# Kernel tuning notes

Hardware: AMD Instinct MI355X
Metric: run time of the kernel (lower is better)

The kernel has to match this reference:

```python
import jax, jax.numpy as jnp
import numpy as np

HEAD_SIZE = 128

def setup_inputs() -> dict:
    key = jax.random.key(0)
    ks = jax.random.split(key, 4)
    B, T, C, H = 8, 2048, 1024, HEAD_SIZE
    x = jax.random.normal(ks[0], (B, T, C), dtype=jnp.float32)
    Wk = jax.random.normal(ks[1], (C, H), dtype=jnp.float32) * (C ** -0.5)
    Wq = jax.random.normal(ks[2], (C, H), dtype=jnp.float32) * (C ** -0.5)
    Wv = jax.random.normal(ks[3], (C, H), dtype=jnp.float32) * (C ** -0.5)
    return {"x": x, "Wk": Wk, "Wq": Wq, "Wv": Wv}

def reference(x, Wk, Wq, Wv):
    # x: [B,T,C]; projections to [B,T,H]
    k = jnp.einsum('btc,ch->bth', x, Wk)
    q = jnp.einsum('btc,ch->bth', x, Wq)
    v = jnp.einsum('btc,ch->bth', x, Wv)
    scale = HEAD_SIZE ** -0.5
    wei = jnp.einsum('bqh,bkh->bqk', q, k) * scale  # [B,T,T]
    T = x.shape[1]
    causal = jnp.tril(jnp.ones((T, T), dtype=bool))
    wei = jnp.where(causal, wei, -jnp.inf)
    wei = jax.nn.softmax(wei, axis=-1)
    # dropout p=0 (eval) -> identity
    out = jnp.einsum('bqk,bkh->bqh', wei, v)  # [B,T,H]
    return out
```

## Files before the change

### kernel.cpp

```cpp
#include <hip/hip_runtime.h>

#define B_DIM 8
#define T_DIM 2048
#define C_DIM 1024
#define H_DIM 128

typedef __attribute__((ext_vector_type(8))) short bf16x8;
typedef __attribute__((ext_vector_type(4))) float f32x4;

__device__ __forceinline__ short f2bf(float f) {
  union { float f; unsigned u; } v; v.f = f;
  unsigned u = v.u;
  unsigned r = (u + 0x7FFFu + ((u >> 16) & 1u)) >> 16;
  return (short)r;
}

__device__ __forceinline__ void gload_lds16(const short* g, short* l) {
  __builtin_amdgcn_global_load_lds(
      (const __attribute__((address_space(1))) void*)g,
      (__attribute__((address_space(3))) void*)l, 16, 0, 0);
}

__device__ __forceinline__ float rowmax16(float x) {
  union { float f; int i; } a, t;
  a.f = x;
  t.i = __builtin_amdgcn_update_dpp(a.i, a.i, 0x128, 0xf, 0xf, false);
  a.f = fmaxf(a.f, t.f);
  t.i = __builtin_amdgcn_update_dpp(a.i, a.i, 0x124, 0xf, 0xf, false);
  a.f = fmaxf(a.f, t.f);
  t.i = __builtin_amdgcn_update_dpp(a.i, a.i, 0x122, 0xf, 0xf, false);
  a.f = fmaxf(a.f, t.f);
  t.i = __builtin_amdgcn_update_dpp(a.i, a.i, 0x121, 0xf, 0xf, false);
  a.f = fmaxf(a.f, t.f);
  return a.f;
}
__device__ __forceinline__ float rowsum16(float x) {
  union { float f; int i; } a, t;
  a.f = x;
  t.i = __builtin_amdgcn_update_dpp(a.i, a.i, 0x128, 0xf, 0xf, false);
  a.f += t.f;
  t.i = __builtin_amdgcn_update_dpp(a.i, a.i, 0x124, 0xf, 0xf, false);
  a.f += t.f;
  t.i = __builtin_amdgcn_update_dpp(a.i, a.i, 0x122, 0xf, 0xf, false);
  a.f += t.f;
  t.i = __builtin_amdgcn_update_dpp(a.i, a.i, 0x121, 0xf, 0xf, false);
  a.f += t.f;
  return a.f;
}

#define NXE ((B_DIM * T_DIM * C_DIM) / 8)
#define NWE ((3 * C_DIM * H_DIM) / 8)

__global__ __launch_bounds__(256) void prep_kernel(
    const float* __restrict__ x, const float* __restrict__ Wk,
    const float* __restrict__ Wq, const float* __restrict__ Wv,
    short* __restrict__ xb, short* __restrict__ Wt) {
  int gid = blockIdx.x * 256 + threadIdx.x;
  if (gid < NXE) {
    const float* src = x + (size_t)gid * 8;
    float4 f0 = ((const float4*)src)[0];
    float4 f1 = ((const float4*)src)[1];
    __attribute__((aligned(16))) short t[8];
    t[0] = f2bf(f0.x); t[1] = f2bf(f0.y); t[2] = f2bf(f0.z); t[3] = f2bf(f0.w);
    t[4] = f2bf(f1.x); t[5] = f2bf(f1.y); t[6] = f2bf(f1.z); t[7] = f2bf(f1.w);
    ((int4*)xb)[gid] = *(const int4*)t;
  } else {
    int j = gid - NXE;
    if (j >= NWE) return;
    int w = j >> 14;
    int r = j & 16383;
    int h = r >> 7;
    int c0 = (r & 127) * 8;
    const float* W = (w == 0) ? Wk : ((w == 1) ? Wq : Wv);
    __attribute__((aligned(16))) short t[8];
#pragma unroll
    for (int i = 0; i < 8; i++) t[i] = f2bf(W[(size_t)(c0 + i) * H_DIM + h]);
    *(int4*)(Wt + (size_t)w * (C_DIM * H_DIM) + h * C_DIM + c0) = *(const int4*)t;
  }
}

__global__ __launch_bounds__(256) void proj_kernel(
    const short* __restrict__ xb, const short* __restrict__ Wt,
    short* __restrict__ Kp, short* __restrict__ Qb, short* __restrict__ Vp) {
  const int wi = blockIdx.y;
  const int m0 = blockIdx.x * 128;
  __shared__ short As[128 * 32];
  __shared__ short Bs[128 * 32];
  const int tid  = threadIdx.x;
  const int lane = tid & 63;
  const int wv   = tid >> 6;
  const int n    = lane & 15;
  const int quad = lane >> 4;
  const int mbase = (wv >> 1) * 64;
  const int nbase = (wv & 1) * 64;
  const short* Wp = Wt + (size_t)wi * (C_DIM * H_DIM);

  const int lr = lane >> 2;
  const int lc = (lane & 3) * 8;

  f32x4 acc[4][4];
#pragma unroll
  for (int i = 0; i < 4; i++)
#pragma unroll
    for (int j = 0; j < 4; j++) {
      f32x4 z = {0.f, 0.f, 0.f, 0.f};
      acc[i][j] = z;
    }

  for (int k0 = 0; k0 < C_DIM; k0 += 32) {
    __syncthreads();
#pragma unroll
    for (int h = 0; h < 2; h++) {
      int ch = wv * 2 + h;
      int row = ch * 16 + lr;
      gload_lds16(xb + (size_t)(m0 + row) * C_DIM + k0 + lc, &As[ch * 512]);
      gload_lds16(Wp + (size_t)row * C_DIM + k0 + lc, &Bs[ch * 512]);
    }
    __syncthreads();

    bf16x8 aF[4], bF[4];
#pragma unroll
    for (int mt = 0; mt < 4; mt++)
      aF[mt] = *(const bf16x8*)&As[(mbase + mt * 16 + n) * 32 + quad * 8];
#pragma unroll
    for (int nt = 0; nt < 4; nt++)
      bF[nt] = *(const bf16x8*)&Bs[(nbase + nt * 16 + n) * 32 + quad * 8];
#pragma unroll
    for (int mt = 0; mt < 4; mt++)
#pragma unroll
      for (int nt = 0; nt < 4; nt++)
        acc[mt][nt] = __builtin_amdgcn_mfma_f32_16x16x32_bf16(
            aF[mt], bF[nt], acc[mt][nt], 0, 0, 0);
  }

#pragma unroll
  for (int mt = 0; mt < 4; mt++) {
#pragma unroll
    for (int nt = 0; nt < 4; nt++) {
#pragma unroll
      for (int i = 0; i < 4; i++) {
        int row = m0 + mbase + mt * 16 + quad * 4 + i;
        int col = nbase + nt * 16 + n;
        short v = f2bf(acc[mt][nt][i]);
        int bb = row >> 11;
        int t  = row & (T_DIM - 1);
        int tt = t >> 6;
        if (wi == 0) {
          int rr = t & 63;
          int knt = rr >> 4, kn = rr & 15;
          int kc = col >> 5, kq = (col >> 3) & 3, kj = col & 7;
          Kp[(((size_t)(bb * 32 + tt) * 16 + knt * 4 + kc) * 512) +
             (kq * 16 + kn) * 8 + kj] = v;
        } else if (wi == 1) {
          Qb[(size_t)row * H_DIM + col] = v;
        } else {
          int vkc = (t >> 5) & 1, vq = (t >> 3) & 3, vj = t & 7;
          int ht = col >> 4, vn = col & 15;
          Vp[(((size_t)(bb * 32 + tt) * 16 + ht * 2 + vkc) * 512) +
             (vq * 16 + vn) * 8 + vj] = v;
        }
      }
    }
  }
}

__global__ __launch_bounds__(256, 4) void attn_kernel(
    const short* __restrict__ Qb, const short* __restrict__ Kp,
    const short* __restrict__ Vp, float* __restrict__ out) {
  const int id = blockIdx.y * 128 + blockIdx.x;
  const int b  = id & 7;
  const int qt = id >> 3;
  const int q0 = qt * 16;
  const int tid  = threadIdx.x;
  const int lane = tid & 63;
  const int g    = tid >> 6;
  const int n    = lane & 15;
  const int quad = lane >> 4;

  __shared__ short Ps[4][16][72];
  __shared__ float Om[16][128];
  __shared__ float Ml[16][2];

  const int ntiles = (qt >> 2) + 1;
  const float scale = 0.08838834764831845f;
  const int row0 = q0 + quad * 4;

  const short* Kbase = Kp + (size_t)b * 32 * 16 * 512;
  const short* Vbase = Vp + (size_t)b * 32 * 16 * 512;

  bf16x8 aQ[4];
  {
    const short* qrow = Qb + (size_t)(b * T_DIM + q0 + n) * H_DIM;
#pragma unroll
    for (int kc = 0; kc < 4; kc++)
      aQ[kc] = *(const bf16x8*)(qrow + kc * 32 + quad * 8);
  }

  f32x4 accO[8];
#pragma unroll
  for (int i = 0; i < 8; i++) {
    f32x4 z = {0.f, 0.f, 0.f, 0.f};
    accO[i] = z;
  }
  float mrow[4] = {-1e30f, -1e30f, -1e30f, -1e30f};
  float lrow[4] = {0.f, 0.f, 0.f, 0.f};

  for (int t = g; t < ntiles; t += 4) {
    const int j0 = t * 64;
    const short* Kt = Kbase + (size_t)t * 16 * 512 + lane * 8;
    const short* Vt = Vbase + (size_t)t * 16 * 512 + lane * 8;
    f32x4 accS[4];
#pragma unroll
    for (int nt = 0; nt < 4; nt++) {
      f32x4 z = {0.f, 0.f, 0.f, 0.f};
      accS[nt] = z;
    }
    bf16x8 fr[8];
#pragma unroll
    for (int nt = 0; nt < 2; nt++)
#pragma unroll
      for (int kc = 0; kc < 4; kc++)
        fr[nt * 4 + kc] = *(const bf16x8*)(Kt + (nt * 4 + kc) * 512);
    __builtin_amdgcn_sched_barrier(0);
#pragma unroll
    for (int nt = 0; nt < 2; nt++)
#pragma unroll
      for (int kc = 0; kc < 4; kc++)
        accS[nt] = __builtin_amdgcn_mfma_f32_16x16x32_bf16(
            aQ[kc], fr[nt * 4 + kc], accS[nt], 0, 0, 0);
    __builtin_amdgcn_sched_barrier(0);
#pragma unroll
    for (int nt = 0; nt < 2; nt++)
#pragma unroll
      for (int kc = 0; kc < 4; kc++)
        fr[nt * 4 + kc] = *(const bf16x8*)(Kt + ((nt + 2) * 4 + kc) * 512);
    __builtin_amdgcn_sched_barrier(0);
#pragma unroll
    for (int nt = 0; nt < 2; nt++)
#pragma unroll
      for (int kc = 0; kc < 4; kc++)
        accS[nt + 2] = __builtin_amdgcn_mfma_f32_16x16x32_bf16(
            aQ[kc], fr[nt * 4 + kc], accS[nt + 2], 0, 0, 0);
    __builtin_amdgcn_sched_barrier(0);

    float mt4[4] = {-1e30f, -1e30f, -1e30f, -1e30f};
#pragma unroll
    for (int nt = 0; nt < 4; nt++) {
      int col = j0 + nt * 16 + n;
#pragma unroll
      for (int i = 0; i < 4; i++) {
        float s = accS[nt][i] * scale;
        s = (col > row0 + i) ? -1e30f : s;
        accS[nt][i] = s;
        mt4[i] = fmaxf(mt4[i], s);
      }
    }
#pragma unroll
    for (int i = 0; i < 4; i++) mt4[i] = rowmax16(mt4[i]);

    bf16x8 frv[8];
#pragma unroll
    for (int ht = 0; ht < 4; ht++)
#pragma unroll
      for (int kc = 0; kc < 2; kc++)
        frv[ht * 2 + kc] = *(const bf16x8*)(Vt + (ht * 2 + kc) * 512);
    __builtin_amdgcn_sched_barrier(0);

    float alpha[4], rsum[4];
#pragma unroll
    for (int i = 0; i < 4; i++) {
      float mnew = fmaxf(mrow[i], mt4[i]);
      alpha[i] = __expf(mrow[i] - mnew);
      mrow[i] = mnew;
      rsum[i] = 0.f;
    }
#pragma unroll
    for (int nt = 0; nt < 4; nt++)
#pragma unroll
      for (int i = 0; i < 4; i++) {
        float p = __expf(accS[nt][i] - mrow[i]);
        rsum[i] += p;
        Ps[g][quad * 4 + i][nt * 16 + n] = f2bf(p);
      }
#pragma unroll
    for (int i = 0; i < 4; i++) {
      rsum[i] = rowsum16(rsum[i]);
      lrow[i] = lrow[i] * alpha[i] + rsum[i];
    }
#pragma unroll
    for (int ht = 0; ht < 8; ht++)
#pragma unroll
      for (int i = 0; i < 4; i++)
        accO[ht][i] *= alpha[i];

    asm volatile("s_waitcnt lgkmcnt(0)" ::: "memory");
    __builtin_amdgcn_sched_barrier(0);

    bf16x8 aP[2];
#pragma unroll
    for (int kc = 0; kc < 2; kc++)
      aP[kc] = *(const bf16x8*)&Ps[g][n][kc * 32 + quad * 8];

#pragma unroll
    for (int ht = 0; ht < 4; ht++)
#pragma unroll
      for (int kc = 0; kc < 2; kc++)
        accO[ht] = __builtin_amdgcn_mfma_f32_16x16x32_bf16(
            aP[kc], frv[ht * 2 + kc], accO[ht], 0, 0, 0);
    __builtin_amdgcn_sched_barrier(0);
#pragma unroll
    for (int ht = 0; ht < 4; ht++)
#pragma unroll
      for (int kc = 0; kc < 2; kc++)
        frv[ht * 2 + kc] = *(const bf16x8*)(Vt + ((ht + 4) * 2 + kc) * 512);
    __builtin_amdgcn_sched_barrier(0);
#pragma unroll
    for (int ht = 0; ht < 4; ht++)
#pragma unroll
      for (int kc = 0; kc < 2; kc++)
        accO[ht + 4] = __builtin_amdgcn_mfma_f32_16x16x32_bf16(
            aP[kc], frv[ht * 2 + kc], accO[ht + 4], 0, 0, 0);
  }

  __syncthreads();
  if (g == 0) {
#pragma unroll
    for (int i = 0; i < 4; i++) {
      int r = quad * 4 + i;
#pragma unroll
      for (int ht = 0; ht < 8; ht++)
        Om[r][ht * 16 + n] = accO[ht][i];
      if (n == 0) { Ml[r][0] = mrow[i]; Ml[r][1] = lrow[i]; }
    }
  }
#pragma unroll
  for (int gg = 1; gg < 4; gg++) {
    __syncthreads();
    if (g == gg) {
#pragma unroll
      for (int i = 0; i < 4; i++) {
        int r = quad * 4 + i;
        float m1 = Ml[r][0], l1 = Ml[r][1];
        float mnew = fmaxf(mrow[i], m1);
        float a0 = __expf(mrow[i] - mnew);
        float a1 = __expf(m1 - mnew);
        float lnew = lrow[i] * a0 + l1 * a1;
        if (gg < 3) {
          if (n == 0) { Ml[r][0] = mnew; Ml[r][1] = lnew; }
#pragma unroll
          for (int ht = 0; ht < 8; ht++)
            Om[r][ht * 16 + n] = accO[ht][i] * a0 + Om[r][ht * 16 + n] * a1;
        } else {
          float linv = 1.0f / lnew;
          size_t base = (size_t)(b * T_DIM + q0 + r) * H_DIM;
#pragma unroll
          for (int ht = 0; ht < 8; ht++)
            out[base + ht * 16 + n] =
                (accO[ht][i] * a0 + Om[r][ht * 16 + n] * a1) * linv;
        }
      }
    }
  }
}

extern "C" void kernel_launch(void* const* d_in, const int* in_sizes, int n_in,
                              void* d_out, int out_size, void* d_ws, size_t ws_size,
                              hipStream_t stream) {
  (void)in_sizes; (void)n_in; (void)out_size; (void)ws_size;
  const float* x  = (const float*)d_in[0];
  const float* Wk = (const float*)d_in[1];
  const float* Wq = (const float*)d_in[2];
  const float* Wv = (const float*)d_in[3];
  float* out = (float*)d_out;

  char* ws = (char*)d_ws;
  short* Wt = (short*)ws;
  short* Kp = (short*)(ws + 786432);
  short* Qb = (short*)(ws + 786432 + 4194304);
  short* Vp = (short*)(ws + 786432 + 8388608);
  short* xb = (short*)(ws + 786432 + 12582912);

  prep_kernel<<<dim3((NXE + NWE) / 256), dim3(256), 0, stream>>>(x, Wk, Wq, Wv, xb, Wt);
  proj_kernel<<<dim3(128, 3), dim3(256), 0, stream>>>(xb, Wt, Kp, Qb, Vp);
  attn_kernel<<<dim3(128, 8), dim3(256), 0, stream>>>(Qb, Kp, Vp, out);
}
```

Measured before the change: 178.5 us.

## Fuse x bf16 conversion into a single QKV projection kernel and reorder attention blocks

Removes the separate pass that converted all of x to bf16 in workspace. The new projection kernel reads fp32 x directly, converts it in registers, and computes K, Q and V together in one kernel with 384 output columns per block, using swizzled LDS for the weights. This avoids writing and re-reading a 32 MB bf16 copy of x and reads x once instead of three times, at the cost of a larger LDS footprint and only 256 blocks. The attention kernel also launches the longest causal query tiles first, loads all 16 K fragments before its MFMAs, and relaxes launch bounds to 2 blocks per SM to leave room for the extra registers.

```diff
diff --git a/kernel.cpp b/kernel.cpp
--- a/kernel.cpp
+++ b/kernel.cpp
@@ -48,114 +48,123 @@
   return a.f;
 }
 
-#define NXE ((B_DIM * T_DIM * C_DIM) / 8)
 #define NWE ((3 * C_DIM * H_DIM) / 8)
 
-__global__ __launch_bounds__(256) void prep_kernel(
-    const float* __restrict__ x, const float* __restrict__ Wk,
-    const float* __restrict__ Wq, const float* __restrict__ Wv,
-    short* __restrict__ xb, short* __restrict__ Wt) {
-  int gid = blockIdx.x * 256 + threadIdx.x;
-  if (gid < NXE) {
-    const float* src = x + (size_t)gid * 8;
-    float4 f0 = ((const float4*)src)[0];
-    float4 f1 = ((const float4*)src)[1];
-    __attribute__((aligned(16))) short t[8];
-    t[0] = f2bf(f0.x); t[1] = f2bf(f0.y); t[2] = f2bf(f0.z); t[3] = f2bf(f0.w);
-    t[4] = f2bf(f1.x); t[5] = f2bf(f1.y); t[6] = f2bf(f1.z); t[7] = f2bf(f1.w);
-    ((int4*)xb)[gid] = *(const int4*)t;
-  } else {
-    int j = gid - NXE;
-    if (j >= NWE) return;
-    int w = j >> 14;
-    int r = j & 16383;
-    int h = r >> 7;
-    int c0 = (r & 127) * 8;
-    const float* W = (w == 0) ? Wk : ((w == 1) ? Wq : Wv);
-    __attribute__((aligned(16))) short t[8];
-#pragma unroll
-    for (int i = 0; i < 8; i++) t[i] = f2bf(W[(size_t)(c0 + i) * H_DIM + h]);
-    *(int4*)(Wt + (size_t)w * (C_DIM * H_DIM) + h * C_DIM + c0) = *(const int4*)t;
-  }
-}
-
-__global__ __launch_bounds__(256) void proj_kernel(
-    const short* __restrict__ xb, const short* __restrict__ Wt,
+__global__ __launch_bounds__(256) void wprep_kernel(
+    const float* __restrict__ Wk, const float* __restrict__ Wq,
+    const float* __restrict__ Wv, short* __restrict__ Wt) {
+  int j = blockIdx.x * 256 + threadIdx.x;
+  if (j >= NWE) return;
+  int w = j >> 14;
+  int r = j & 16383;
+  int h = r >> 7;
+  int c0 = (r & 127) * 8;
+  const float* W = (w == 0) ? Wk : ((w == 1) ? Wq : Wv);
+  __attribute__((aligned(16))) short t[8];
+#pragma unroll
+  for (int i = 0; i < 8; i++) t[i] = f2bf(W[(size_t)(c0 + i) * H_DIM + h]);
+  *(int4*)(Wt + (size_t)w * (C_DIM * H_DIM) + h * C_DIM + c0) = *(const int4*)t;
+}
+
+__global__ __launch_bounds__(512, 2) void projf_kernel(
+    const float* __restrict__ x, const short* __restrict__ Wt,
     short* __restrict__ Kp, short* __restrict__ Qb, short* __restrict__ Vp) {
-  const int wi = blockIdx.y;
-  const int m0 = blockIdx.x * 128;
-  __shared__ short As[128 * 32];
-  __shared__ short Bs[128 * 32];
+  const int m0 = blockIdx.x * 64;
+  __shared__ short As[64][72];
+  __shared__ short Bs[384 * 64];
   const int tid  = threadIdx.x;
   const int lane = tid & 63;
   const int wv   = tid >> 6;
   const int n    = lane & 15;
   const int quad = lane >> 4;
-  const int mbase = (wv >> 1) * 64;
-  const int nbase = (wv & 1) * 64;
-  const short* Wp = Wt + (size_t)wi * (C_DIM * H_DIM);
-
-  const int lr = lane >> 2;
-  const int lc = (lane & 3) * 8;
-
-  f32x4 acc[4][4];
-#pragma unroll
-  for (int i = 0; i < 4; i++)
-#pragma unroll
-    for (int j = 0; j < 4; j++) {
+  const int mh = wv >> 2;
+  const int nq = wv & 3;
+
+  const int ar = tid >> 3, ac = (tid & 7) * 8;
+  const float* xrow = x + (size_t)(m0 + ar) * C_DIM + ac;
+  const int brl = lane >> 3;
+  const int bce = 8 * ((lane & 7) ^ brl);
+
+  f32x4 acc[2][6];
+#pragma unroll
+  for (int i = 0; i < 2; i++)
+#pragma unroll
+    for (int j = 0; j < 6; j++) {
       f32x4 z = {0.f, 0.f, 0.f, 0.f};
       acc[i][j] = z;
     }
 
-  for (int k0 = 0; k0 < C_DIM; k0 += 32) {
+  float4 ax0, ax1;
+  auto LOADA = [&](int k0) {
+    ax0 = *(const float4*)(xrow + k0);
+    ax1 = *(const float4*)(xrow + k0 + 4);
+  };
+  auto STOREA = [&]() {
+    __attribute__((aligned(16))) short t8[8];
+    t8[0] = f2bf(ax0.x); t8[1] = f2bf(ax0.y); t8[2] = f2bf(ax0.z); t8[3] = f2bf(ax0.w);
+    t8[4] = f2bf(ax1.x); t8[5] = f2bf(ax1.y); t8[6] = f2bf(ax1.z); t8[7] = f2bf(ax1.w);
+    *(int4*)&As[ar][ac] = *(const int4*)t8;
+  };
+
+  LOADA(0);
+  for (int it = 0; it < 16; it++) {
+    const int k0 = it * 64;
     __syncthreads();
 #pragma unroll
-    for (int h = 0; h < 2; h++) {
-      int ch = wv * 2 + h;
-      int row = ch * 16 + lr;
-      gload_lds16(xb + (size_t)(m0 + row) * C_DIM + k0 + lc, &As[ch * 512]);
-      gload_lds16(Wp + (size_t)row * C_DIM + k0 + lc, &Bs[ch * 512]);
-    }
+    for (int h = 0; h < 6; h++) {
+      int c = wv * 6 + h;
+      gload_lds16(Wt + (size_t)(c * 8 + brl) * C_DIM + k0 + bce, &Bs[c * 512]);
+    }
+    STOREA();
+    if (it < 15) LOADA(k0 + 64);
     __syncthreads();
 
-    bf16x8 aF[4], bF[4];
-#pragma unroll
-    for (int mt = 0; mt < 4; mt++)
-      aF[mt] = *(const bf16x8*)&As[(mbase + mt * 16 + n) * 32 + quad * 8];
-#pragma unroll
-    for (int nt = 0; nt < 4; nt++)
-      bF[nt] = *(const bf16x8*)&Bs[(nbase + nt * 16 + n) * 32 + quad * 8];
-#pragma unroll
-    for (int mt = 0; mt < 4; mt++)
-#pragma unroll
-      for (int nt = 0; nt < 4; nt++)
-        acc[mt][nt] = __builtin_amdgcn_mfma_f32_16x16x32_bf16(
-            aF[mt], bF[nt], acc[mt][nt], 0, 0, 0);
-  }
-
-#pragma unroll
-  for (int mt = 0; mt < 4; mt++) {
-#pragma unroll
-    for (int nt = 0; nt < 4; nt++) {
+#pragma unroll
+    for (int kk = 0; kk < 2; kk++) {
+      bf16x8 aF[2], bF[6];
+#pragma unroll
+      for (int mt = 0; mt < 2; mt++)
+        aF[mt] = *(const bf16x8*)&As[mh * 32 + mt * 16 + n][kk * 32 + quad * 8];
+#pragma unroll
+      for (int nt = 0; nt < 6; nt++) {
+        int row = nq * 96 + nt * 16 + n;
+        int off = (kk * 64 + quad * 16) ^ ((row & 7) << 4);
+        bF[nt] = *(const bf16x8*)((const char*)&Bs[row * 64] + off);
+      }
+#pragma unroll
+      for (int mt = 0; mt < 2; mt++)
+#pragma unroll
+        for (int nt = 0; nt < 6; nt++)
+          acc[mt][nt] = __builtin_amdgcn_mfma_f32_16x16x32_bf16(
+              aF[mt], bF[nt], acc[mt][nt], 0, 0, 0);
+    }
+  }
+
+#pragma unroll
+  for (int mt = 0; mt < 2; mt++) {
+#pragma unroll
+    for (int nt = 0; nt < 6; nt++) {
 #pragma unroll
       for (int i = 0; i < 4; i++) {
-        int row = m0 + mbase + mt * 16 + quad * 4 + i;
-        int col = nbase + nt * 16 + n;
+        int row = m0 + mh * 32 + mt * 16 + quad * 4 + i;
+        int col = nq * 96 + nt * 16 + n;
         short v = f2bf(acc[mt][nt][i]);
+        int w = col >> 7;
+        int c = col & 127;
         int bb = row >> 11;
         int t  = row & (T_DIM - 1);
         int tt = t >> 6;
-        if (wi == 0) {
+        if (w == 0) {
           int rr = t & 63;
           int knt = rr >> 4, kn = rr & 15;
-          int kc = col >> 5, kq = (col >> 3) & 3, kj = col & 7;
+          int kc = c >> 5, kq = (c >> 3) & 3, kj = c & 7;
           Kp[(((size_t)(bb * 32 + tt) * 16 + knt * 4 + kc) * 512) +
              (kq * 16 + kn) * 8 + kj] = v;
-        } else if (wi == 1) {
-          Qb[(size_t)row * H_DIM + col] = v;
+        } else if (w == 1) {
+          Qb[(size_t)row * H_DIM + c] = v;
         } else {
           int vkc = (t >> 5) & 1, vq = (t >> 3) & 3, vj = t & 7;
-          int ht = col >> 4, vn = col & 15;
+          int ht = c >> 4, vn = c & 15;
           Vp[(((size_t)(bb * 32 + tt) * 16 + ht * 2 + vkc) * 512) +
              (vq * 16 + vn) * 8 + vj] = v;
         }
@@ -164,12 +173,12 @@
   }
 }
 
-__global__ __launch_bounds__(256, 4) void attn_kernel(
+__global__ __launch_bounds__(256, 2) void attn_kernel(
     const short* __restrict__ Qb, const short* __restrict__ Kp,
     const short* __restrict__ Vp, float* __restrict__ out) {
   const int id = blockIdx.y * 128 + blockIdx.x;
   const int b  = id & 7;
-  const int qt = id >> 3;
+  const int qt = 127 - (id >> 3);
   const int q0 = qt * 16;
   const int tid  = threadIdx.x;
   const int lane = tid & 63;
@@ -215,32 +224,19 @@
       f32x4 z = {0.f, 0.f, 0.f, 0.f};
       accS[nt] = z;
     }
-    bf16x8 fr[8];
-#pragma unroll
-    for (int nt = 0; nt < 2; nt++)
+    bf16x8 fr[16];
+#pragma unroll
+    for (int nt = 0; nt < 4; nt++)
 #pragma unroll
       for (int kc = 0; kc < 4; kc++)
         fr[nt * 4 + kc] = *(const bf16x8*)(Kt + (nt * 4 + kc) * 512);
     __builtin_amdgcn_sched_barrier(0);
 #pragma unroll
-    for (int nt = 0; nt < 2; nt++)
+    for (int nt = 0; nt < 4; nt++)
 #pragma unroll
       for (int kc = 0; kc < 4; kc++)
         accS[nt] = __builtin_amdgcn_mfma_f32_16x16x32_bf16(
             aQ[kc], fr[nt * 4 + kc], accS[nt], 0, 0, 0);
-    __builtin_amdgcn_sched_barrier(0);
-#pragma unroll
-    for (int nt = 0; nt < 2; nt++)
-#pragma unroll
-      for (int kc = 0; kc < 4; kc++)
-        fr[nt * 4 + kc] = *(const bf16x8*)(Kt + ((nt + 2) * 4 + kc) * 512);
-    __builtin_amdgcn_sched_barrier(0);
-#pragma unroll
-    for (int nt = 0; nt < 2; nt++)
-#pragma unroll
-      for (int kc = 0; kc < 4; kc++)
-        accS[nt + 2] = __builtin_amdgcn_mfma_f32_16x16x32_bf16(
-            aQ[kc], fr[nt * 4 + kc], accS[nt + 2], 0, 0, 0);
     __builtin_amdgcn_sched_barrier(0);
 
     float mt4[4] = {-1e30f, -1e30f, -1e30f, -1e30f};
@@ -378,9 +374,8 @@
   short* Kp = (short*)(ws + 786432);
   short* Qb = (short*)(ws + 786432 + 4194304);
   short* Vp = (short*)(ws + 786432 + 8388608);
-  short* xb = (short*)(ws + 786432 + 12582912);
-
-  prep_kernel<<<dim3((NXE + NWE) / 256), dim3(256), 0, stream>>>(x, Wk, Wq, Wv, xb, Wt);
-  proj_kernel<<<dim3(128, 3), dim3(256), 0, stream>>>(xb, Wt, Kp, Qb, Vp);
+
+  wprep_kernel<<<dim3(192), dim3(256), 0, stream>>>(Wk, Wq, Wv, Wt);
+  projf_kernel<<<dim3(256), dim3(512), 0, stream>>>(x, Wt, Kp, Qb, Vp);
   attn_kernel<<<dim3(128, 8), dim3(256), 0, stream>>>(Qb, Kp, Vp, out);
 }
```

After: 159.9 us. -10.4%, faster.
